# Optimization experiments

Hardware: AMD Instinct MI355X
Metric: run time of the kernel (lower is better)

## Reference

```python
import jax, jax.numpy as jnp
import numpy as np

B, T, C, H = 8, 2048, 1024, 64

def setup_inputs() -> dict:
    key = jax.random.key(0)
    kx, kq, kk, kv = jax.random.split(key, 4)
    scale = 1.0 / np.sqrt(C)
    return {
        "x": jax.random.normal(kx, (B, T, C), dtype=jnp.float32),
        "Wq": jax.random.normal(kq, (C, H), dtype=jnp.float32) * scale,
        "Wk": jax.random.normal(kk, (C, H), dtype=jnp.float32) * scale,
        "Wv": jax.random.normal(kv, (C, H), dtype=jnp.float32) * scale,
    }

def reference(x, Wq, Wk, Wv):
    # q,k,v: [B,T,H]
    q = jnp.einsum('btc,ch->bth', x, Wq)
    k = jnp.einsum('btc,ch->bth', x, Wk)
    v = jnp.einsum('btc,ch->bth', x, Wv)
    scale = k.shape[-1] ** -0.5
    wei = jnp.einsum('bth,bsh->bts', q, k) * scale  # [B,T,T]
    causal = jnp.tril(jnp.ones((x.shape[1], x.shape[1]), dtype=bool))
    wei = jnp.where(causal, wei, -jnp.inf)
    wei = jax.nn.softmax(wei, axis=-1)
    out = jnp.einsum('bts,bsh->bth', wei, v)  # [B,T,H]
    return out
```

## Files before the change

kernel.cpp:

```cpp
#include <hip/hip_runtime.h>

#define B_ 8
#define T_ 2048
#define C_ 1024
#define H_ 64

typedef __bf16 bf16x8 __attribute__((ext_vector_type(8)));
typedef float  f32x4  __attribute__((ext_vector_type(4)));
typedef unsigned short u16x8 __attribute__((ext_vector_type(8)));

__device__ __forceinline__ unsigned short f2bf(float f) {
    unsigned u = __builtin_bit_cast(unsigned, f);
    u += 0x8000u;
    return (unsigned short)(u >> 16);
}

__device__ __forceinline__ float bf2f(unsigned short v) {
    unsigned u = ((unsigned)v) << 16;
    return __builtin_bit_cast(float, u);
}

__device__ __forceinline__ unsigned pack2(float lo, float hi) {
    unsigned a = __builtin_bit_cast(unsigned, lo) + 0x8000u;
    unsigned b = __builtin_bit_cast(unsigned, hi) + 0x8000u;
    return (a >> 16) | (b & 0xffff0000u);
}

union U8 { unsigned u32[4]; u16x8 v; };

__device__ __forceinline__ u16x8 cvt8(float4 f0, float4 f1) {
    U8 r;
    r.u32[0] = pack2(f0.x, f0.y);
    r.u32[1] = pack2(f0.z, f0.w);
    r.u32[2] = pack2(f1.x, f1.y);
    r.u32[3] = pack2(f1.z, f1.w);
    return r.v;
}

__device__ __forceinline__ bf16x8 load8_bf(const unsigned short* p) {
    return __builtin_bit_cast(bf16x8, *(const u16x8*)p);
}


__global__ void cast_weights(const float* __restrict__ Wq,
                             const float* __restrict__ Wk,
                             const float* __restrict__ Wv,
                             unsigned short* __restrict__ Wtf) {
    int idx = blockIdx.x * blockDim.x + threadIdx.x;
    int n   = idx % 192;
    int c   = idx / 192;
    int w   = n >> 6;
    int h   = n & 63;
    const float* W = (w == 0) ? Wq : (w == 1) ? Wk : Wv;
    int nt = n >> 4, l16 = n & 15;
    int kk = c >> 5, quad = (c >> 3) & 3, j = c & 7;
    Wtf[(size_t)(nt * 32 + kk) * 512 + l16 * 32 + quad * 8 + j] =
        f2bf(W[(size_t)c * H_ + h]);
}

__global__ __launch_bounds__(256) void qkv_proj(
        const float* __restrict__ x,
        const unsigned short* __restrict__ Wtf,
        unsigned short* __restrict__ Qf,
        unsigned short* __restrict__ Kf,
        unsigned short* __restrict__ Vf) {
    __shared__ __attribute__((aligned(16))) unsigned short As_[32 * 512];

    const int tid  = threadIdx.x;
    const int ns   = tid >> 6;
    const int lane = tid & 63;
    const int l16  = lane & 15;
    const int quad = lane >> 4;
    const size_t r0 = (size_t)blockIdx.x * 32;
    const int bb    = (int)(r0 >> 11);
    const int tloc0 = (int)(r0 & (T_ - 1));
    const int t16_0 = tloc0 >> 4;
    const int s32   = tloc0 >> 5;

    f32x4 acc[6];
#pragma unroll
    for (int i = 0; i < 6; i++) acc[i] = (f32x4){0.f, 0.f, 0.f, 0.f};

    const int sw   = l16 & 7;
    const int loff = l16 * 32 + quad * 8;

    for (int p = 0; p < 2; p++) {
        if (p) __syncthreads();
#pragma unroll
        for (int i = 0; i < 8; i++) {
            int c   = i * 256 + tid;
            int row = c >> 6;
            int g   = c & 63;
            const float* sp = x + (r0 + row) * C_ + p * 512 + g * 8;
            float4 f0 = *(const float4*)sp;
            float4 f1 = *(const float4*)(sp + 4);
            int off = row * 512 + ((g & ~7) + ((g & 7) ^ (row & 7))) * 8;
            *(u16x8*)(&As_[off]) = cvt8(f0, f1);
        }
        __syncthreads();

#pragma unroll 4
        for (int kc = 0; kc < 16; kc++) {
            int g  = kc * 4 + quad;
            int gs = ((g & ~7) + ((g & 7) ^ sw)) * 8;
            bf16x8 a0 = load8_bf(&As_[l16 * 512 + gs]);
            bf16x8 a1 = load8_bf(&As_[(16 + l16) * 512 + gs]);
            int kk = p * 16 + kc;
#pragma unroll
            for (int i = 0; i < 3; i++) {
                bf16x8 b = load8_bf(Wtf + (size_t)((ns * 3 + i) * 32 + kk) * 512 + loff);
                acc[i]     = __builtin_amdgcn_mfma_f32_16x16x32_bf16(a0, b, acc[i],     0, 0, 0);
                acc[3 + i] = __builtin_amdgcn_mfma_f32_16x16x32_bf16(a1, b, acc[3 + i], 0, 0, 0);
            }
        }
    }

    __syncthreads();
    unsigned short* E = As_;
#pragma unroll
    for (int i = 0; i < 3; i++) {
        int nt = ns * 3 + i;
#pragma unroll
        for (int msI = 0; msI < 2; msI++) {
#pragma unroll
            for (int r = 0; r < 4; r++) {
                unsigned short bv = f2bf(acc[msI * 3 + i][r]);
                int off;
                int ch;
                if (nt < 4) {
                    ch  = msI * 2 + (nt >> 1);
                    off = (quad * 4 + r) * 32 + ((nt & 1) * 2 + (l16 >> 3)) * 8 + (l16 & 7);
                } else if (nt < 8) {
                    int nk = nt - 4;
                    ch  = 4 + msI * 2 + (nk >> 1);
                    off = (quad * 4 + r) * 32 + ((nk & 1) * 2 + (l16 >> 3)) * 8 + (l16 & 7);
                } else {
                    int w32 = msI * 16 + quad * 4 + r;
                    ch  = 8 + (nt - 8);
                    off = l16 * 32 + (w32 >> 3) * 8 + (w32 & 7);
                }
                E[ch * 512 + off] = bv;
            }
        }
    }
    __syncthreads();

#pragma unroll
    for (int i = 0; i < 3; i++) {
        int gi = i * 256 + tid;
        int ch = gi >> 6;
        int g  = gi & 63;
        unsigned short* dst;
        if (ch < 4) {
            dst = Qf + ((size_t)(bb * 128 + t16_0 + (ch >> 1)) * 2 + (ch & 1)) * 512;
        } else if (ch < 8) {
            int c2 = ch - 4;
            dst = Kf + ((size_t)(bb * 128 + t16_0 + (c2 >> 1)) * 2 + (c2 & 1)) * 512;
        } else {
            dst = Vf + ((size_t)(bb * 64 + s32) * 4 + (ch - 8)) * 512;
        }
        *(u16x8*)(dst + g * 8) = *(const u16x8*)(&E[ch * 512 + g * 8]);
    }
}

#define PROW 33
#define OMS2 66

__global__ __launch_bounds__(256) void attn(
        const unsigned short* __restrict__ Qf,
        const unsigned short* __restrict__ Kf,
        const unsigned short* __restrict__ Vf,
        float* __restrict__ out) {
    __shared__ unsigned int ps_[4 * 32 * PROW];
    __shared__ unsigned short Om_[4 * 32 * OMS2];
    __shared__ float mred_[4][32];
    __shared__ float lred_[4][32];

    const int tid  = threadIdx.x;
    const int wave = tid >> 6;
    const int lane = tid & 63;
    const int l16  = lane & 15;
    const int quad = lane >> 4;
    const int b    = blockIdx.x & 7;
    const int qt32 = blockIdx.x >> 3;
    const int q0   = qt32 * 32;
    const int tdiag = qt32 >> 1;

    const int loff = l16 * 32 + quad * 8;

    bf16x8 qf[2][2];
#pragma unroll
    for (int qg = 0; qg < 2; qg++) {
        const unsigned short* Qfb = Qf + (size_t)((b * 128 + qt32 * 2 + qg) * 2) * 512;
        qf[qg][0] = load8_bf(Qfb + loff);
        qf[qg][1] = load8_bf(Qfb + 512 + loff);
    }

    f32x4 o[8];
#pragma unroll
    for (int i = 0; i < 8; i++) o[i] = (f32x4){0.f, 0.f, 0.f, 0.f};
    float m_run[2] = {-1e30f, -1e30f}, l_run[2] = {0.f, 0.f};

    const float scale = 0.125f;
    const unsigned short* Kfb = Kf + (size_t)b * 128 * 1024;
    const unsigned short* Vfb = Vf + (size_t)b * 64 * 2048;
    unsigned int* Pw = &ps_[wave * 32 * PROW];

    for (int t = wave; t <= tdiag; t += 4) {
        bf16x8 vf[8];
#pragma unroll
        for (int ks = 0; ks < 2; ks++)
#pragma unroll
            for (int ht = 0; ht < 4; ht++)
                vf[ht * 2 + ks] = load8_bf(
                    Vfb + ((size_t)(t * 2 + ks) * 4 + ht) * 512 + loff);

        f32x4 s[2][4];
#pragma unroll
        for (int nt = 0; nt < 4; nt++) {
            const unsigned short* kp = Kfb + (size_t)(t * 4 + nt) * 1024;
            bf16x8 kf0 = load8_bf(kp + loff);
            bf16x8 kf1 = load8_bf(kp + 512 + loff);
#pragma unroll
            for (int qg = 0; qg < 2; qg++) {
                f32x4 z = (f32x4){0.f, 0.f, 0.f, 0.f};
                z = __builtin_amdgcn_mfma_f32_16x16x32_bf16(kf0, qf[qg][0], z, 0, 0, 0);
                z = __builtin_amdgcn_mfma_f32_16x16x32_bf16(kf1, qf[qg][1], z, 0, 0, 0);
                s[qg][nt] = z;
            }
        }

#pragma unroll
        for (int qg = 0; qg < 2; qg++)
#pragma unroll
            for (int nt = 0; nt < 4; nt++)
#pragma unroll
                for (int r = 0; r < 4; r++) s[qg][nt][r] *= scale;

        if (t == tdiag) {
#pragma unroll
            for (int qg = 0; qg < 2; qg++) {
                int q = q0 + qg * 16 + l16;
#pragma unroll
                for (int nt = 0; nt < 4; nt++)
#pragma unroll
                    for (int r = 0; r < 4; r++) {
                        int key = t * 64 + nt * 16 + quad * 4 + r;
                        if (key > q) s[qg][nt][r] = -1e30f;
                    }
            }
        }

#pragma unroll
        for (int qg = 0; qg < 2; qg++) {
            float m0 = fmaxf(fmaxf(s[qg][0][0], s[qg][0][1]), fmaxf(s[qg][0][2], s[qg][0][3]));
            float m1 = fmaxf(fmaxf(s[qg][1][0], s[qg][1][1]), fmaxf(s[qg][1][2], s[qg][1][3]));
            float m2 = fmaxf(fmaxf(s[qg][2][0], s[qg][2][1]), fmaxf(s[qg][2][2], s[qg][2][3]));
            float m3 = fmaxf(fmaxf(s[qg][3][0], s[qg][3][1]), fmaxf(s[qg][3][2], s[qg][3][3]));
            float mx = fmaxf(fmaxf(m0, m1), fmaxf(m2, m3));
            mx = fmaxf(mx, __shfl_xor(mx, 16));
            mx = fmaxf(mx, __shfl_xor(mx, 32));
            const float m_new = fmaxf(m_run[qg], mx);
            const float alpha = __expf(m_run[qg] - m_new);
            m_run[qg] = m_new;

            float rs = 0.f;
#pragma unroll
            for (int nt = 0; nt < 4; nt++) {
#pragma unroll
                for (int i = 0; i < 2; i++) {
                    float p0 = __expf(s[qg][nt][2 * i]     - m_new);
                    float p1 = __expf(s[qg][nt][2 * i + 1] - m_new);
                    rs += p0 + p1;
                    Pw[(qg * 16 + l16) * PROW + nt * 8 + quad * 2 + i] = pack2(p0, p1);
                }
            }
            rs += __shfl_xor(rs, 16);
            rs += __shfl_xor(rs, 32);
            l_run[qg] = l_run[qg] * alpha + rs;

#pragma unroll
            for (int ht = 0; ht < 4; ht++)
#pragma unroll
                for (int r = 0; r < 4; r++) o[qg * 4 + ht][r] *= alpha;
        }

#pragma unroll
        for (int ks = 0; ks < 2; ks++) {
#pragma unroll
            for (int qg = 0; qg < 2; qg++) {
                bf16x8 pB = __builtin_bit_cast(bf16x8,
                    *(const u16x8*)(&Pw[(qg * 16 + l16) * PROW + ks * 16 + quad * 4]));
#pragma unroll
                for (int ht = 0; ht < 4; ht++)
                    o[qg * 4 + ht] = __builtin_amdgcn_mfma_f32_16x16x32_bf16(
                        vf[ht * 2 + ks], pB, o[qg * 4 + ht], 0, 0, 0);
            }
        }
    }

#pragma unroll
    for (int qg = 0; qg < 2; qg++) {
#pragma unroll
        for (int ht = 0; ht < 4; ht++)
#pragma unroll
            for (int r = 0; r < 4; r++)
                Om_[(wave * 32 + qg * 16 + l16) * OMS2 + ht * 16 + quad * 4 + r] =
                    f2bf(o[qg * 4 + ht][r]);
        if (quad == 0) {
            mred_[wave][qg * 16 + l16] = m_run[qg];
            lred_[wave][qg * 16 + l16] = l_run[qg];
        }
    }
    __syncthreads();

    const int hcol = tid & 63;
    const int qr0  = tid >> 6;
#pragma unroll
    for (int qq = 0; qq < 8; qq++) {
        const int q = qr0 + qq * 4;
        float M = -1e30f;
#pragma unroll
        for (int w = 0; w < 4; w++) M = fmaxf(M, mred_[w][q]);
        float lt = 0.f, ov = 0.f;
#pragma unroll
        for (int w = 0; w < 4; w++) {
            float e = __expf(mred_[w][q] - M);
            lt += e * lred_[w][q];
            ov += e * bf2f(Om_[(w * 32 + q) * OMS2 + hcol]);
        }
        out[((size_t)b * T_ + q0 + q) * H_ + hcol] = ov / lt;
    }
}

extern "C" void kernel_launch(void* const* d_in, const int* in_sizes, int n_in,
                              void* d_out, int out_size, void* d_ws, size_t ws_size,
                              hipStream_t stream) {
    const float* x  = (const float*)d_in[0];
    const float* Wq = (const float*)d_in[1];
    const float* Wk = (const float*)d_in[2];
    const float* Wv = (const float*)d_in[3];
    float* out = (float*)d_out;

    unsigned short* Qf  = (unsigned short*)d_ws;
    unsigned short* Kf  = Qf + (size_t)B_ * T_ * H_;
    unsigned short* Vf  = Kf + (size_t)B_ * T_ * H_;
    unsigned short* Wtf = Vf + (size_t)B_ * T_ * H_;

    cast_weights<<<(192 * C_) / 256, 256, 0, stream>>>(Wq, Wk, Wv, Wtf);
    qkv_proj<<<B_ * T_ / 32, 256, 0, stream>>>(x, Wtf, Qf, Kf, Vf);
    attn<<<B_ * (T_ / 32), 256, 0, stream>>>(Qf, Kf, Vf, out);
}
```

Before: 142.7 us.

## Halve QKV projection row tile to 16 and load full K dimension at once

The QKV projection now handles 16 rows per block instead of 32, which doubles the grid to 1024 blocks. Each block stages all 1024 input columns in LDS in a single pass instead of two half passes. The epilogue is reworked so V tiles are written as 16-row halves into the 32-row V fragment layout. The aim is more parallelism and occupancy (launch bounds hint 4 blocks), at the cost of each weight fragment being reused across fewer rows, so total weight traffic from L2 doubles.

```diff
diff --git a/kernel.cpp b/kernel.cpp
--- a/kernel.cpp
+++ b/kernel.cpp
@@ -58,60 +58,55 @@
         f2bf(W[(size_t)c * H_ + h]);
 }
 
-__global__ __launch_bounds__(256) void qkv_proj(
+__global__ __launch_bounds__(256, 4) void qkv_proj(
         const float* __restrict__ x,
         const unsigned short* __restrict__ Wtf,
         unsigned short* __restrict__ Qf,
         unsigned short* __restrict__ Kf,
         unsigned short* __restrict__ Vf) {
-    __shared__ __attribute__((aligned(16))) unsigned short As_[32 * 512];
+    __shared__ __attribute__((aligned(16))) unsigned short As_[16 * 1024];
 
     const int tid  = threadIdx.x;
     const int ns   = tid >> 6;
     const int lane = tid & 63;
     const int l16  = lane & 15;
     const int quad = lane >> 4;
-    const size_t r0 = (size_t)blockIdx.x * 32;
-    const int bb    = (int)(r0 >> 11);
-    const int tloc0 = (int)(r0 & (T_ - 1));
-    const int t16_0 = tloc0 >> 4;
-    const int s32   = tloc0 >> 5;
-
-    f32x4 acc[6];
-#pragma unroll
-    for (int i = 0; i < 6; i++) acc[i] = (f32x4){0.f, 0.f, 0.f, 0.f};
+    const size_t r0 = (size_t)blockIdx.x * 16;
+    const int bb     = (int)(r0 >> 11);
+    const int tloc0  = (int)(r0 & (T_ - 1));
+    const int t16_0  = tloc0 >> 4;
+    const int s32    = tloc0 >> 5;
+    const int half16 = t16_0 & 1;
+
+    f32x4 acc[3];
+#pragma unroll
+    for (int i = 0; i < 3; i++) acc[i] = (f32x4){0.f, 0.f, 0.f, 0.f};
 
     const int sw   = l16 & 7;
     const int loff = l16 * 32 + quad * 8;
 
-    for (int p = 0; p < 2; p++) {
-        if (p) __syncthreads();
-#pragma unroll
-        for (int i = 0; i < 8; i++) {
-            int c   = i * 256 + tid;
-            int row = c >> 6;
-            int g   = c & 63;
-            const float* sp = x + (r0 + row) * C_ + p * 512 + g * 8;
-            float4 f0 = *(const float4*)sp;
-            float4 f1 = *(const float4*)(sp + 4);
-            int off = row * 512 + ((g & ~7) + ((g & 7) ^ (row & 7))) * 8;
-            *(u16x8*)(&As_[off]) = cvt8(f0, f1);
-        }
-        __syncthreads();
+#pragma unroll
+    for (int i = 0; i < 8; i++) {
+        int c   = i * 256 + tid;
+        int row = c >> 7;
+        int g   = c & 127;
+        const float* sp = x + (r0 + row) * C_ + g * 8;
+        float4 f0 = *(const float4*)sp;
+        float4 f1 = *(const float4*)(sp + 4);
+        int off = row * 1024 + ((g & ~7) + ((g & 7) ^ (row & 7))) * 8;
+        *(u16x8*)(&As_[off]) = cvt8(f0, f1);
+    }
+    __syncthreads();
 
 #pragma unroll 4
-        for (int kc = 0; kc < 16; kc++) {
-            int g  = kc * 4 + quad;
-            int gs = ((g & ~7) + ((g & 7) ^ sw)) * 8;
-            bf16x8 a0 = load8_bf(&As_[l16 * 512 + gs]);
-            bf16x8 a1 = load8_bf(&As_[(16 + l16) * 512 + gs]);
-            int kk = p * 16 + kc;
-#pragma unroll
-            for (int i = 0; i < 3; i++) {
-                bf16x8 b = load8_bf(Wtf + (size_t)((ns * 3 + i) * 32 + kk) * 512 + loff);
-                acc[i]     = __builtin_amdgcn_mfma_f32_16x16x32_bf16(a0, b, acc[i],     0, 0, 0);
-                acc[3 + i] = __builtin_amdgcn_mfma_f32_16x16x32_bf16(a1, b, acc[3 + i], 0, 0, 0);
-            }
+    for (int kk = 0; kk < 32; kk++) {
+        int g  = kk * 4 + quad;
+        int gs = ((g & ~7) + ((g & 7) ^ sw)) * 8;
+        bf16x8 a0 = load8_bf(&As_[l16 * 1024 + gs]);
+#pragma unroll
+        for (int i = 0; i < 3; i++) {
+            bf16x8 b = load8_bf(Wtf + (size_t)((ns * 3 + i) * 32 + kk) * 512 + loff);
+            acc[i] = __builtin_amdgcn_mfma_f32_16x16x32_bf16(a0, b, acc[i], 0, 0, 0);
         }
     }
 
@@ -121,45 +116,41 @@
     for (int i = 0; i < 3; i++) {
         int nt = ns * 3 + i;
 #pragma unroll
-        for (int msI = 0; msI < 2; msI++) {
-#pragma unroll
-            for (int r = 0; r < 4; r++) {
-                unsigned short bv = f2bf(acc[msI * 3 + i][r]);
-                int off;
-                int ch;
-                if (nt < 4) {
-                    ch  = msI * 2 + (nt >> 1);
-                    off = (quad * 4 + r) * 32 + ((nt & 1) * 2 + (l16 >> 3)) * 8 + (l16 & 7);
-                } else if (nt < 8) {
-                    int nk = nt - 4;
-                    ch  = 4 + msI * 2 + (nk >> 1);
-                    off = (quad * 4 + r) * 32 + ((nk & 1) * 2 + (l16 >> 3)) * 8 + (l16 & 7);
-                } else {
-                    int w32 = msI * 16 + quad * 4 + r;
-                    ch  = 8 + (nt - 8);
-                    off = l16 * 32 + (w32 >> 3) * 8 + (w32 & 7);
-                }
-                E[ch * 512 + off] = bv;
-            }
+        for (int r = 0; r < 4; r++) {
+            unsigned short bv = f2bf(acc[i][r]);
+            int off;
+            if (nt < 4) {
+                off = (nt >> 1) * 512 + (quad * 4 + r) * 32 +
+                      ((nt & 1) * 2 + (l16 >> 3)) * 8 + (l16 & 7);
+            } else if (nt < 8) {
+                int nk = nt - 4;
+                off = 1024 + (nk >> 1) * 512 + (quad * 4 + r) * 32 +
+                      ((nk & 1) * 2 + (l16 >> 3)) * 8 + (l16 & 7);
+            } else {
+                int ht = nt - 8;
+                off = 2048 + ht * 256 + l16 * 16 + quad * 4 + r;
+            }
+            E[off] = bv;
         }
     }
     __syncthreads();
 
-#pragma unroll
-    for (int i = 0; i < 3; i++) {
-        int gi = i * 256 + tid;
-        int ch = gi >> 6;
-        int g  = gi & 63;
-        unsigned short* dst;
-        if (ch < 4) {
-            dst = Qf + ((size_t)(bb * 128 + t16_0 + (ch >> 1)) * 2 + (ch & 1)) * 512;
-        } else if (ch < 8) {
-            int c2 = ch - 4;
-            dst = Kf + ((size_t)(bb * 128 + t16_0 + (c2 >> 1)) * 2 + (c2 & 1)) * 512;
-        } else {
-            dst = Vf + ((size_t)(bb * 64 + s32) * 4 + (ch - 8)) * 512;
-        }
+    {
+        int ch = tid >> 6;
+        int g  = tid & 63;
+        unsigned short* dst = (ch < 2) ? Qf : Kf;
+        int part = ch & 1;
+        dst += ((size_t)(bb * 128 + t16_0) * 2 + part) * 512;
         *(u16x8*)(dst + g * 8) = *(const u16x8*)(&E[ch * 512 + g * 8]);
+    }
+    if (tid < 128) {
+        int ht   = tid >> 5;
+        int rr   = tid & 31;
+        int l16v = rr >> 1;
+        int hh   = rr & 1;
+        unsigned short* dst = Vf + ((size_t)(bb * 64 + s32) * 4 + ht) * 512
+                              + l16v * 32 + half16 * 16 + hh * 8;
+        *(u16x8*)dst = *(const u16x8*)(&E[2048 + ht * 256 + l16v * 16 + hh * 8]);
     }
 }
 
@@ -348,6 +339,6 @@
     unsigned short* Wtf = Vf + (size_t)B_ * T_ * H_;
 
     cast_weights<<<(192 * C_) / 256, 256, 0, stream>>>(Wq, Wk, Wv, Wtf);
-    qkv_proj<<<B_ * T_ / 32, 256, 0, stream>>>(x, Wtf, Qf, Kf, Vf);
+    qkv_proj<<<B_ * T_ / 16, 256, 0, stream>>>(x, Wtf, Qf, Kf, Vf);
     attn<<<B_ * (T_ / 32), 256, 0, stream>>>(Qf, Kf, Vf, out);
 }
```

Measured after the change: 139.6 us. -2.2%, faster.

## Load x fragments directly from global in QKV projection, drop LDS staging

Applied to the files above, without the earlier changes.

The QKV projection no longer stages the fp32 x tile into shared memory. Each wave instead reads its MFMA A-operand straight from global memory and converts it to bf16 in registers. Waves are repartitioned into 2 row strips by 2 column halves of 6 output tiles each, the epilogue LDS buffer shrinks, and launch bounds request 3 blocks per SIMD for occupancy. The aim is to remove the LDS round trip and the barriers between staging and compute. In exchange, the x loads become strided per lane with less coalescing, and the x rows are read by two waves.

```diff
diff --git a/kernel.cpp b/kernel.cpp
--- a/kernel.cpp
+++ b/kernel.cpp
@@ -58,19 +58,21 @@
         f2bf(W[(size_t)c * H_ + h]);
 }
 
-__global__ __launch_bounds__(256) void qkv_proj(
+__global__ __launch_bounds__(256, 3) void qkv_proj(
         const float* __restrict__ x,
         const unsigned short* __restrict__ Wtf,
         unsigned short* __restrict__ Qf,
         unsigned short* __restrict__ Kf,
         unsigned short* __restrict__ Vf) {
-    __shared__ __attribute__((aligned(16))) unsigned short As_[32 * 512];
-
-    const int tid  = threadIdx.x;
-    const int ns   = tid >> 6;
-    const int lane = tid & 63;
-    const int l16  = lane & 15;
-    const int quad = lane >> 4;
+    __shared__ __attribute__((aligned(16))) unsigned short E[12 * 512];
+
+    const int tid   = threadIdx.x;
+    const int w     = tid >> 6;
+    const int strip = w & 1;
+    const int nh    = w >> 1;
+    const int lane  = tid & 63;
+    const int l16   = lane & 15;
+    const int quad  = lane >> 4;
     const size_t r0 = (size_t)blockIdx.x * 32;
     const int bb    = (int)(r0 >> 11);
     const int tloc0 = (int)(r0 & (T_ - 1));
@@ -81,73 +83,48 @@
 #pragma unroll
     for (int i = 0; i < 6; i++) acc[i] = (f32x4){0.f, 0.f, 0.f, 0.f};
 
-    const int sw   = l16 & 7;
-    const int loff = l16 * 32 + quad * 8;
-
-    for (int p = 0; p < 2; p++) {
-        if (p) __syncthreads();
-#pragma unroll
-        for (int i = 0; i < 8; i++) {
-            int c   = i * 256 + tid;
-            int row = c >> 6;
-            int g   = c & 63;
-            const float* sp = x + (r0 + row) * C_ + p * 512 + g * 8;
-            float4 f0 = *(const float4*)sp;
-            float4 f1 = *(const float4*)(sp + 4);
-            int off = row * 512 + ((g & ~7) + ((g & 7) ^ (row & 7))) * 8;
-            *(u16x8*)(&As_[off]) = cvt8(f0, f1);
-        }
-        __syncthreads();
-
-#pragma unroll 4
-        for (int kc = 0; kc < 16; kc++) {
-            int g  = kc * 4 + quad;
-            int gs = ((g & ~7) + ((g & 7) ^ sw)) * 8;
-            bf16x8 a0 = load8_bf(&As_[l16 * 512 + gs]);
-            bf16x8 a1 = load8_bf(&As_[(16 + l16) * 512 + gs]);
-            int kk = p * 16 + kc;
-#pragma unroll
-            for (int i = 0; i < 3; i++) {
-                bf16x8 b = load8_bf(Wtf + (size_t)((ns * 3 + i) * 32 + kk) * 512 + loff);
-                acc[i]     = __builtin_amdgcn_mfma_f32_16x16x32_bf16(a0, b, acc[i],     0, 0, 0);
-                acc[3 + i] = __builtin_amdgcn_mfma_f32_16x16x32_bf16(a1, b, acc[3 + i], 0, 0, 0);
-            }
-        }
-    }
-
+    const float* xp = x + (r0 + strip * 16 + l16) * C_ + quad * 8;
+    const unsigned short* wp = Wtf + (size_t)(nh * 6 * 32) * 512
+                               + l16 * 32 + quad * 8;
+
+#pragma unroll 2
+    for (int kk = 0; kk < 32; kk++) {
+        float4 f0 = *(const float4*)(xp + kk * 32);
+        float4 f1 = *(const float4*)(xp + kk * 32 + 4);
+        bf16x8 a0 = __builtin_bit_cast(bf16x8, cvt8(f0, f1));
+#pragma unroll
+        for (int i = 0; i < 6; i++) {
+            bf16x8 b = load8_bf(wp + (size_t)(i * 32 + kk) * 512);
+            acc[i] = __builtin_amdgcn_mfma_f32_16x16x32_bf16(a0, b, acc[i], 0, 0, 0);
+        }
+    }
+
+#pragma unroll
+    for (int i = 0; i < 6; i++) {
+        int nt = nh * 6 + i;
+#pragma unroll
+        for (int r = 0; r < 4; r++) {
+            unsigned short bv = f2bf(acc[i][r]);
+            int off;
+            if (nt < 4) {
+                off = (strip * 2 + (nt >> 1)) * 512 +
+                      (quad * 4 + r) * 32 + (nt & 1) * 16 + l16;
+            } else if (nt < 8) {
+                int nk = nt - 4;
+                off = 2048 + (strip * 2 + (nk >> 1)) * 512 +
+                      (quad * 4 + r) * 32 + (nk & 1) * 16 + l16;
+            } else {
+                int ht = nt - 8;
+                off = 4096 + ht * 512 + l16 * 32 + strip * 16 + quad * 4 + r;
+            }
+            E[off] = bv;
+        }
+    }
     __syncthreads();
-    unsigned short* E = As_;
-#pragma unroll
-    for (int i = 0; i < 3; i++) {
-        int nt = ns * 3 + i;
-#pragma unroll
-        for (int msI = 0; msI < 2; msI++) {
-#pragma unroll
-            for (int r = 0; r < 4; r++) {
-                unsigned short bv = f2bf(acc[msI * 3 + i][r]);
-                int off;
-                int ch;
-                if (nt < 4) {
-                    ch  = msI * 2 + (nt >> 1);
-                    off = (quad * 4 + r) * 32 + ((nt & 1) * 2 + (l16 >> 3)) * 8 + (l16 & 7);
-                } else if (nt < 8) {
-                    int nk = nt - 4;
-                    ch  = 4 + msI * 2 + (nk >> 1);
-                    off = (quad * 4 + r) * 32 + ((nk & 1) * 2 + (l16 >> 3)) * 8 + (l16 & 7);
-                } else {
-                    int w32 = msI * 16 + quad * 4 + r;
-                    ch  = 8 + (nt - 8);
-                    off = l16 * 32 + (w32 >> 3) * 8 + (w32 & 7);
-                }
-                E[ch * 512 + off] = bv;
-            }
-        }
-    }
-    __syncthreads();
-
-#pragma unroll
-    for (int i = 0; i < 3; i++) {
-        int gi = i * 256 + tid;
+
+#pragma unroll
+    for (int c3 = 0; c3 < 3; c3++) {
+        int gi = c3 * 256 + tid;
         int ch = gi >> 6;
         int g  = gi & 63;
         unsigned short* dst;
```

Measured after the change: 168.9 us. 18.3% more time.
